# Optimization experiments

Measured on AMD Instinct MI355X. Metric: run time of the kernel, lower is better.

Reference implementation:

```python
import jax, jax.numpy as jnp
import numpy as np

B, H, W, DM = 4, 64, 64, 96
DS, DC, K = 16, 3, 4
DI = DM            # expand = 1.0
DTR = 6            # ceil(96/16)


def setup_inputs() -> dict:
    key = jax.random.key(0)
    ks = jax.random.split(key, 12)
    s = 0.02
    # dt bias init exactly as MS2D.dt_init: dt ~ exp(U*(log(max)-log(min))+log(min)); inv softplus
    dt = jnp.exp(jax.random.uniform(ks[5], (K, DI)) * (np.log(0.1) - np.log(0.001)) + np.log(0.001))
    dt = jnp.clip(dt, 1e-4, None)
    inv_dt = dt + jnp.log(-jnp.expm1(-dt))
    A_logs = jnp.log(jnp.broadcast_to(jnp.arange(1, DS + 1, dtype=jnp.float32), (K, DI, DS)))
    return {
        "x": jax.random.normal(ks[0], (B, H, W, DM), jnp.float32),
        "in_proj_w": jax.random.normal(ks[1], (2 * DI, DM), jnp.float32) * s,
        "conv_w": jax.random.normal(ks[2], (DI, 1, DC, DC), jnp.float32) * s,
        "conv_b": jnp.zeros((DI,), jnp.float32),
        "x_proj_weight": jax.random.normal(ks[3], (K, DTR + 2 * DS, DI), jnp.float32) * s,
        "dt_projs_weight": jax.random.uniform(ks[4], (K, DI, DTR), minval=-1.0, maxval=1.0) * (DTR ** -0.5),
        "dt_projs_bias": inv_dt,
        "A_logs": A_logs,
        "Ds": jnp.ones((K, DI), jnp.float32),
        "out_norm_w": jnp.ones((DI,), jnp.float32),
        "out_norm_b": jnp.zeros((DI,), jnp.float32),
        "out_proj_w": jax.random.normal(ks[6], (DM, DI), jnp.float32) * s,
    }


def _ms2d(x, in_proj_w, conv_w, conv_b, x_proj_weight, dt_projs_weight,
          dt_projs_bias, A_logs, Ds, out_norm_w, out_norm_b, out_proj_w):
    Bb, Hh, Ww, _ = x.shape
    L = Hh * Ww
    # in_proj -> (x, z) gating split
    xz = x @ in_proj_w.T                      # (B,H,W,2*DI)
    xc, z = jnp.split(xz, 2, axis=-1)
    xc = jnp.transpose(xc, (0, 3, 1, 2))      # (B,DI,H,W)
    xc = jax.lax.conv_general_dilated(
        xc, conv_w, (1, 1), 'SAME', feature_group_count=xc.shape[1],
        dimension_numbers=('NCHW', 'OIHW', 'NCHW')) + conv_b[None, :, None, None]
    xc = jax.nn.silu(xc)
    d = xc.shape[1]
    # 4-directional scan sequences: hw, wh, and their reverses
    x_hw = xc.reshape(Bb, d, L)
    x_wh = jnp.transpose(xc, (0, 1, 3, 2)).reshape(Bb, d, L)
    x2 = jnp.stack([x_hw, x_wh], axis=1)          # (B,2,d,L)
    xs = jnp.concatenate([x2, jnp.flip(x2, axis=-1)], axis=1)  # (B,4,d,L)
    x_dbl = jnp.einsum('bkdl,kcd->bkcl', xs, x_proj_weight)
    dtr = dt_projs_weight.shape[2]
    n = A_logs.shape[2]
    dts, Bs, Cs = jnp.split(x_dbl, [dtr, dtr + n], axis=2)     # (B,4,r,L),(B,4,N,L),(B,4,N,L)
    dts = jnp.einsum('bkrl,kdr->bkdl', dts, dt_projs_weight)
    delta = jax.nn.softplus(dts + dt_projs_bias[None, :, :, None])  # (B,4,d,L)
    A = -jnp.exp(A_logs)                                        # (4,d,N)
    # time-major for scan
    u_t = jnp.moveaxis(xs, -1, 0)       # (L,B,4,d)
    dl_t = jnp.moveaxis(delta, -1, 0)
    B_t = jnp.moveaxis(Bs, -1, 0)       # (L,B,4,N)
    C_t = jnp.moveaxis(Cs, -1, 0)

    def step(h, inp):                   # h: (B,4,d,N)
        u, dl, b, c = inp
        dA = jnp.exp(dl[..., None] * A)
        h = h * dA + (dl * u)[..., None] * b[:, :, None, :]
        y = jnp.einsum('bkdn,bkn->bkd', h, c)
        return h, y

    h0 = jnp.zeros((Bb, 4, d, n), xs.dtype)
    _, ys = jax.lax.scan(step, h0, (u_t, dl_t, B_t, C_t))
    ys = jnp.moveaxis(ys, 0, -1)        # (B,4,d,L)
    ys = ys + Ds[None, :, :, None] * xs  # skip D*u
    inv_y = jnp.flip(ys[:, 2:4], axis=-1)

    def wh2hw(t):  # undo the (W,H) raster order
        return jnp.transpose(t.reshape(Bb, d, Ww, Hh), (0, 1, 3, 2)).reshape(Bb, d, L)

    y = ys[:, 0] + inv_y[:, 0] + wh2hw(ys[:, 1]) + wh2hw(inv_y[:, 1])
    y = jnp.transpose(y, (0, 2, 1)).reshape(Bb, Hh, Ww, d)
    mu = y.mean(-1, keepdims=True)
    var = y.var(-1, keepdims=True)
    y = (y - mu) / jnp.sqrt(var + 1e-5) * out_norm_w + out_norm_b
    y = y * jax.nn.silu(z)
    return y @ out_proj_w.T


def reference(x, in_proj_w, conv_w, conv_b, x_proj_weight, dt_projs_weight,
              dt_projs_bias, A_logs, Ds, out_norm_w, out_norm_b, out_proj_w):
    return _ms2d(x, in_proj_w, conv_w, conv_b, x_proj_weight, dt_projs_weight,
                 dt_projs_bias, A_logs, Ds, out_norm_w, out_norm_b, out_proj_w)
```

## Files before the change

kernel.cpp:

```cpp
#include <hip/hip_runtime.h>
#include <math.h>


#define LQ 4096
#define NCH 128
#define LCH 32

__device__ __forceinline__ float sigmoid_f(float x){ return 1.0f/(1.0f + __expf(-x)); }
__device__ __forceinline__ float silu_f(float x){ return x * sigmoid_f(x); }
__device__ __forceinline__ float softplus_f(float x){ return (x > 20.0f) ? x : __logf(1.0f + __expf(x)); }

__device__ __forceinline__ int pos_of(int k, int i){
  switch(k & 3){
    case 0: return i;
    case 1: return ((i & 63) << 6) | (i >> 6);
    case 2: return LQ - 1 - i;
    default: { int j = LQ - 1 - i; return ((j & 63) << 6) | (j >> 6); }
  }
}

__device__ __forceinline__ void pow8(float r, int nh, float* e){
  e[0]=r; e[1]=r*r; e[2]=e[1]*r; e[3]=e[1]*e[1];
  e[4]=e[3]*r; e[5]=e[3]*e[1]; e[6]=e[3]*e[2]; e[7]=e[3]*e[3];
  float m = nh ? e[7] : 1.0f;
  #pragma unroll
  for (int j=0;j<8;j++) e[j] *= m;
}

__global__ __launch_bounds__(64) void k_prep(const float* __restrict__ Alogs,
                                             float* __restrict__ An_tab,
                                             float* __restrict__ fflag){
  const int t = blockIdx.x*64 + threadIdx.x;
  if (t >= 384) return;
  bool fast = true;
  #pragma unroll
  for (int n=0;n<16;n++){
    float An = -__expf(Alogs[t*16+n]);
    An_tab[t*16+n] = An;
    fast = fast && (fabsf(An + (float)(n+1)) < 1e-3f*(float)(n+1));
  }
  fflag[t] = fast ? 1.0f : 0.0f;
}

__global__ __launch_bounds__(256) void k_inproj(const float* __restrict__ x,
                                                const float* __restrict__ wproj,
                                                float* __restrict__ xc,
                                                float* __restrict__ zb){
  __shared__ float a_s[64*97];
  __shared__ float w_s[96*97];
  const int t = threadIdx.x;
  const int row0 = (blockIdx.x >> 1) * 64;
  const int ch = blockIdx.x & 1;
  for (int e = t*4; e < 64*96; e += 1024){
    float4 v = *(const float4*)(x + (size_t)row0*96 + e);
    int r = e/96, c = e%96;
    float* p = a_s + r*97 + c;
    p[0]=v.x; p[1]=v.y; p[2]=v.z; p[3]=v.w;
  }
  for (int e = t*4; e < 96*96; e += 1024){
    float4 v = *(const float4*)(wproj + (size_t)ch*96*96 + e);
    int r = e/96, c = e%96;
    float* p = w_s + r*97 + c;
    p[0]=v.x; p[1]=v.y; p[2]=v.z; p[3]=v.w;
  }
  __syncthreads();
  const int tr = t >> 5, tc = t & 31;
  float acc[8][3];
  #pragma unroll
  for (int i=0;i<8;i++){
    #pragma unroll
    for (int j=0;j<3;j++) acc[i][j]=0.f;
  }
  for (int kk=0; kk<96; kk++){
    float a[8], b[3];
    #pragma unroll
    for (int i=0;i<8;i++) a[i] = a_s[(tr*8+i)*97+kk];
    #pragma unroll
    for (int j=0;j<3;j++) b[j] = w_s[(tc*3+j)*97+kk];
    #pragma unroll
    for (int i=0;i<8;i++){
      #pragma unroll
      for (int j=0;j<3;j++) acc[i][j] += a[i]*b[j];
    }
  }
  float* dst = ch ? zb : xc;
  #pragma unroll
  for (int i=0;i<8;i++){
    int row = row0 + tr*8 + i;
    #pragma unroll
    for (int j=0;j<3;j++) dst[(size_t)row*96 + tc*3 + j] = acc[i][j];
  }
}

__global__ __launch_bounds__(256) void k_conv(const float* __restrict__ xc,
                                              const float* __restrict__ cw,
                                              const float* __restrict__ cb,
                                              float* __restrict__ u){
  int e = blockIdx.x*256 + threadIdx.x;
  int d0 = (e % 24) * 4;
  int p = e / 24;
  int w = p & 63, h = (p >> 6) & 63, b = p >> 12;
  float cwv[4][9];
  #pragma unroll
  for (int q=0;q<4;q++){
    #pragma unroll
    for (int tp=0;tp<9;tp++) cwv[q][tp] = cw[(d0+q)*9+tp];
  }
  float4 acc = make_float4(cb[d0], cb[d0+1], cb[d0+2], cb[d0+3]);
  #pragma unroll
  for (int kh=0; kh<3; kh++){
    int hh = h + kh - 1;
    if (hh < 0 || hh > 63) continue;
    #pragma unroll
    for (int kw=0; kw<3; kw++){
      int ww = w + kw - 1;
      if (ww < 0 || ww > 63) continue;
      float4 v = *(const float4*)(xc + ((size_t)((b<<12) + (hh<<6) + ww))*96 + d0);
      int tp = kh*3+kw;
      acc.x += v.x*cwv[0][tp]; acc.y += v.y*cwv[1][tp];
      acc.z += v.z*cwv[2][tp]; acc.w += v.w*cwv[3][tp];
    }
  }
  float4 o = make_float4(silu_f(acc.x), silu_f(acc.y), silu_f(acc.z), silu_f(acc.w));
  *(float4*)(u + (size_t)p*96 + d0) = o;
}

__global__ __launch_bounds__(128) void k_proj(const float* __restrict__ u,
                                              const float* __restrict__ xpw,
                                              float* __restrict__ dts,
                                              float* __restrict__ Bsb,
                                              float* __restrict__ Csb,
                                              float* __restrict__ us){
  __shared__ float u_s[64*97];
  __shared__ float w_s[40*97];
  const int t = threadIdx.x;
  const int blk = blockIdx.x;
  const int pt = blk & 63, k = (blk >> 6) & 3, b = blk >> 8;
  const int bk = b*4 + k;
  const int i0 = pt * 64;
  for (int e = t*4; e < 64*96; e += 512){
    int row = e/96, c = e%96;
    int p = pos_of(k, i0 + row);
    float4 v = *(const float4*)(u + ((size_t)((b<<12) + p))*96 + c);
    float* dst = u_s + row*97 + c;
    dst[0]=v.x; dst[1]=v.y; dst[2]=v.z; dst[3]=v.w;
    if (us) *(float4*)(us + ((size_t)((bk<<12) + i0 + row))*96 + c) = v;
  }
  for (int e = t*4; e < 40*96; e += 512){
    int r = e/96, c = e%96;
    float4 v = (r < 38) ? *(const float4*)(xpw + (k*38+r)*96 + c)
                        : make_float4(0,0,0,0);
    float* p = w_s + r*97 + c;
    p[0]=v.x; p[1]=v.y; p[2]=v.z; p[3]=v.w;
  }
  __syncthreads();
  const int posg = t & 15, cg = t >> 4;
  float acc[4][5];
  #pragma unroll
  for (int i=0;i<4;i++){
    #pragma unroll
    for (int j=0;j<5;j++) acc[i][j]=0.f;
  }
  for (int dd=0; dd<96; dd++){
    float uu[4], wv[5];
    #pragma unroll
    for (int i=0;i<4;i++) uu[i] = u_s[(posg*4+i)*97+dd];
    #pragma unroll
    for (int j=0;j<5;j++) wv[j] = w_s[(cg*5+j)*97+dd];
    #pragma unroll
    for (int i=0;i<4;i++){
      #pragma unroll
      for (int j=0;j<5;j++) acc[i][j] += uu[i]*wv[j];
    }
  }
  #pragma unroll
  for (int i=0;i<4;i++){
    int ii = i0 + posg*4 + i;
    int base = (bk<<12) + ii;
    #pragma unroll
    for (int j=0;j<5;j++){
      int c = cg*5 + j;
      float v = acc[i][j];
      if (c < 6)       dts[(size_t)base*6 + c] = v;
      else if (c < 22) Bsb[(size_t)base*16 + (c-6)] = v;
      else if (c < 38) Csb[(size_t)base*16 + (c-22)] = v;
    }
  }
}

__global__ __launch_bounds__(384) void k_scanA2(float* us,
                                                const float* __restrict__ dts,
                                                const float* __restrict__ Bsb,
                                                const float* __restrict__ Csb,
                                                const float* __restrict__ dtw_g,
                                                const float* __restrict__ dtb_g,
                                                const float* __restrict__ An_tab,
                                                const float* __restrict__ fflag,
                                                float* __restrict__ S,
                                                float* __restrict__ sumd,
                                                float* __restrict__ ys){
  const int t = threadIdx.x;
  const int c2 = t / 192;
  const int lane = t & 63;
  const int wv3 = (t % 192) >> 6;
  const int nh = (lane >> 5) & 1;
  const int d = wv3*32 + (lane & 31);
  const int blk = blockIdx.x;
  const int bk = blk >> 6;
  const int k = bk & 3;
  const int chunk = ((blk & 63) << 1) | c2;
  const int ibase = chunk * LCH;
  int wfast = __all(fflag[k*96+d] > 0.5f ? 1 : 0);
  float An[8];
  #pragma unroll
  for (int j=0;j<8;j++) An[j] = An_tab[(k*96+d)*16 + nh*8 + j];
  float dtw[6];
  #pragma unroll
  for (int r=0;r<6;r++) dtw[r] = dtw_g[(k*96+d)*6+r];
  const float bias = dtb_g[k*96+d];
  float* usp = us + ((size_t)((bk<<12)+ibase))*96 + d;
  const float2* dtp = (const float2*)(dts + ((size_t)((bk<<12)+ibase))*6);
  const float4* Bp = (const float4*)(Bsb + ((size_t)((bk<<12)+ibase))*16) + nh*2;
  const float4* Cp = (const float4*)(Csb + ((size_t)((bk<<12)+ibase))*16) + nh*2;
  float* yp = ys + ((size_t)((bk<<12)+ibase))*96 + d;
  float h[8];
  #pragma unroll
  for (int n=0;n<8;n++) h[n]=0.f;
  float cum = 0.f;
  if (wfast){
    #pragma unroll 8
    for (int il=0; il<LCH; il++){
      float uv = usp[(size_t)il*96];
      float2 q0 = dtp[il*3+0], q1 = dtp[il*3+1], q2 = dtp[il*3+2];
      float accd = bias + dtw[0]*q0.x + dtw[1]*q0.y + dtw[2]*q1.x
                        + dtw[3]*q1.y + dtw[4]*q2.x + dtw[5]*q2.y;
      float t1 = __expf(accd);
      float r = 1.0f / (1.0f + t1);
      float delta = (accd > 20.f) ? accd : __logf(1.0f + t1);
      cum += delta;
      float du = delta * uv;
      float4 b0 = Bp[il*4+0], b1 = Bp[il*4+1];
      float4 c0 = Cp[il*4+0], c1 = Cp[il*4+1];
      float Bv[8] = {b0.x,b0.y,b0.z,b0.w, b1.x,b1.y,b1.z,b1.w};
      float Cv[8] = {c0.x,c0.y,c0.z,c0.w, c1.x,c1.y,c1.z,c1.w};
      float e[8];
      pow8(r, nh, e);
      float y8 = 0.f;
      #pragma unroll
      for (int n=0;n<8;n++){
        h[n] = h[n]*e[n] + du*Bv[n];
        y8 += h[n]*Cv[n];
      }
      float y = y8 + __shfl_xor(y8, 32, 64);
      if (nh == 0){ yp[(size_t)il*96] = y; usp[(size_t)il*96] = cum; }
    }
  } else {
    #pragma unroll 2
    for (int il=0; il<LCH; il++){
      float uv = usp[(size_t)il*96];
      float2 q0 = dtp[il*3+0], q1 = dtp[il*3+1], q2 = dtp[il*3+2];
      float accd = bias + dtw[0]*q0.x + dtw[1]*q0.y + dtw[2]*q1.x
                        + dtw[3]*q1.y + dtw[4]*q2.x + dtw[5]*q2.y;
      float delta = softplus_f(accd);
      cum += delta;
      float du = delta * uv;
      float4 b0 = Bp[il*4+0], b1 = Bp[il*4+1];
      float4 c0 = Cp[il*4+0], c1 = Cp[il*4+1];
      float Bv[8] = {b0.x,b0.y,b0.z,b0.w, b1.x,b1.y,b1.z,b1.w};
      float Cv[8] = {c0.x,c0.y,c0.z,c0.w, c1.x,c1.y,c1.z,c1.w};
      float e[8];
      #pragma unroll
      for (int n=0;n<8;n++) e[n] = __expf(delta*An[n]);
      float y8 = 0.f;
      #pragma unroll
      for (int n=0;n<8;n++){
        h[n] = h[n]*e[n] + du*Bv[n];
        y8 += h[n]*Cv[n];
      }
      float y = y8 + __shfl_xor(y8, 32, 64);
      if (nh == 0){ yp[(size_t)il*96] = y; usp[(size_t)il*96] = cum; }
    }
  }
  const int sb = (bk*NCH + chunk)*96 + d;
  float4* Sp = (float4*)(S + (size_t)sb*16 + nh*8);
  Sp[0] = make_float4(h[0],h[1],h[2],h[3]);
  Sp[1] = make_float4(h[4],h[5],h[6],h[7]);
  if (nh == 0) sumd[sb] = cum;
}

__global__ __launch_bounds__(384) void k_scanA_fb(const float* __restrict__ u,
                                                  const float* __restrict__ dts,
                                                  const float* __restrict__ Bsb,
                                                  const float* __restrict__ dtw_g,
                                                  const float* __restrict__ dtb_g,
                                                  const float* __restrict__ Alogs,
                                                  float* __restrict__ S,
                                                  float* __restrict__ sumd){
  const int t = threadIdx.x;
  const int c2 = t / 192;
  const int lane = t & 63;
  const int wv3 = (t % 192) >> 6;
  const int nh = (lane >> 5) & 1;
  const int d = wv3*32 + (lane & 31);
  const int blk = blockIdx.x;
  const int bk = blk >> 6;
  const int k = bk & 3, b = bk >> 2;
  const int chunk = ((blk & 63) << 1) | c2;
  const int ibase = chunk * LCH;
  float An[8];
  bool fast = true;
  #pragma unroll
  for (int j=0;j<8;j++){
    int n = nh*8 + j;
    An[j] = -__expf(Alogs[(k*96+d)*16+n]);
    fast = fast && (fabsf(An[j] + (float)(n+1)) < 1e-3f*(float)(n+1));
  }
  int wfast = __all(fast ? 1 : 0);
  float dtw[6];
  #pragma unroll
  for (int r=0;r<6;r++) dtw[r] = dtw_g[(k*96+d)*6+r];
  const float bias = dtb_g[k*96+d];
  int pb = pos_of(k, ibase);
  int pstep = pos_of(k, ibase+1) - pb;
  const float* uptr = u + ((size_t)((b<<12)+pb))*96 + d;
  const long ustep = (long)pstep*96;
  const float2* dtp = (const float2*)(dts + ((size_t)((bk<<12)+ibase))*6);
  const float4* Bp = (const float4*)(Bsb + ((size_t)((bk<<12)+ibase))*16) + nh*2;
  float h[8];
  #pragma unroll
  for (int n=0;n<8;n++) h[n]=0.f;
  float sdelta = 0.f;
  #pragma unroll 4
  for (int il=0; il<LCH; il++){
    float uv = *uptr;
    float2 q0 = dtp[0], q1 = dtp[1], q2 = dtp[2];
    float accd = bias + dtw[0]*q0.x + dtw[1]*q0.y + dtw[2]*q1.x
                      + dtw[3]*q1.y + dtw[4]*q2.x + dtw[5]*q2.y;
    float t1 = __expf(accd);
    float r = 1.0f / (1.0f + t1);
    float delta = (accd > 20.f) ? accd : __logf(1.0f + t1);
    sdelta += delta;
    float du = delta * uv;
    float4 b0 = Bp[0], b1 = Bp[1];
    float Bv[8] = {b0.x,b0.y,b0.z,b0.w, b1.x,b1.y,b1.z,b1.w};
    float e[8];
    if (wfast){ pow8(r, nh, e); }
    else {
      #pragma unroll
      for (int n=0;n<8;n++) e[n] = __expf(delta*An[n]);
    }
    #pragma unroll
    for (int n=0;n<8;n++) h[n] = h[n]*e[n] + du*Bv[n];
    uptr += ustep; dtp += 3; Bp += 4;
  }
  const int sb = (bk*NCH + chunk)*96 + d;
  float4* Sp = (float4*)(S + (size_t)sb*16 + nh*8);
  Sp[0] = make_float4(h[0],h[1],h[2],h[3]);
  Sp[1] = make_float4(h[4],h[5],h[6],h[7]);
  if (nh == 0) sumd[sb] = sdelta;
}

__global__ __launch_bounds__(128) void k_scanB2(float* __restrict__ S,
                                                const float* __restrict__ sumd,
                                                const float* __restrict__ Alogs,
                                                const float* __restrict__ An_tab,
                                                const float* __restrict__ fflag){
  __shared__ float As[128*17];
  __shared__ float Bs[128*17];
  const int c = threadIdx.x;
  const int blk = blockIdx.x;
  const int d = blk % 96;
  const int bk = blk / 96;
  const int k = bk & 3;
  const int sb = (bk*NCH + c)*96 + d;
  float a[16], bvals[16];
  {
    const float4* Sp = (const float4*)(S + (size_t)sb*16);
    float4 s0=Sp[0], s1=Sp[1], s2=Sp[2], s3=Sp[3];
    bvals[0]=s0.x;bvals[1]=s0.y;bvals[2]=s0.z;bvals[3]=s0.w;
    bvals[4]=s1.x;bvals[5]=s1.y;bvals[6]=s1.z;bvals[7]=s1.w;
    bvals[8]=s2.x;bvals[9]=s2.y;bvals[10]=s2.z;bvals[11]=s2.w;
    bvals[12]=s3.x;bvals[13]=s3.y;bvals[14]=s3.z;bvals[15]=s3.w;
  }
  const float sd = sumd[sb];
  bool fast;
  float An[16];
  if (An_tab){
    fast = fflag[k*96+d] > 0.5f;
    if (!fast){
      #pragma unroll
      for (int n=0;n<16;n++) An[n] = An_tab[(k*96+d)*16+n];
    }
  } else {
    fast = true;
    #pragma unroll
    for (int n=0;n<16;n++){
      An[n] = -__expf(Alogs[(k*96+d)*16+n]);
      fast = fast && (fabsf(An[n] + (float)(n+1)) < 1e-3f*(float)(n+1));
    }
  }
  if (fast){
    float q = __expf(-sd);
    float p = q;
    #pragma unroll
    for (int n=0;n<16;n++){ a[n] = p; p *= q; }
  } else {
    #pragma unroll
    for (int n=0;n<16;n++) a[n] = __expf(An[n]*sd);
  }
  #pragma unroll
  for (int n=0;n<16;n++){ As[c*17+n] = a[n]; Bs[c*17+n] = bvals[n]; }
  for (int dist=1; dist<128; dist<<=1){
    __syncthreads();
    float aL[16], bL[16];
    if (c >= dist){
      #pragma unroll
      for (int n=0;n<16;n++){ aL[n] = As[(c-dist)*17+n]; bL[n] = Bs[(c-dist)*17+n]; }
    }
    __syncthreads();
    if (c >= dist){
      #pragma unroll
      for (int n=0;n<16;n++){
        bvals[n] = bL[n]*a[n] + bvals[n];
        a[n] = aL[n]*a[n];
        As[c*17+n] = a[n]; Bs[c*17+n] = bvals[n];
      }
    }
  }
  __syncthreads();
  float h0[16];
  #pragma unroll
  for (int n=0;n<16;n++) h0[n] = (c == 0) ? 0.f : Bs[(c-1)*17+n];
  float4* Sp = (float4*)(S + (size_t)sb*16);
  Sp[0] = make_float4(h0[0],h0[1],h0[2],h0[3]);
  Sp[1] = make_float4(h0[4],h0[5],h0[6],h0[7]);
  Sp[2] = make_float4(h0[8],h0[9],h0[10],h0[11]);
  Sp[3] = make_float4(h0[12],h0[13],h0[14],h0[15]);
}

__global__ __launch_bounds__(256) void k_scanY(const float* __restrict__ us,
                                               const float* __restrict__ Csb,
                                               const float* __restrict__ An_tab,
                                               const float* __restrict__ fflag,
                                               const float* __restrict__ h0buf,
                                               float* __restrict__ ys){
  __shared__ float h0_s[32*17];
  __shared__ float An_s[32*17];
  __shared__ float ff_s[32];
  const int t = threadIdx.x;
  const int blk = blockIdx.x;
  const int dslice = blk % 3;
  const int tmp = blk / 3;
  const int chunk = tmp & 127;
  const int bk = tmp >> 7;
  const int k = bk & 3;
  const int dbase = dslice * 32;
  {
    const float* h0src = h0buf + ((size_t)((bk*NCH + chunk)*96 + dbase))*16;
    const float* Ansrc = An_tab + (size_t)(k*96 + dbase)*16;
    for (int e = t; e < 512; e += 256){
      int dl = e >> 4, n = e & 15;
      h0_s[dl*17+n] = h0src[e];
      An_s[dl*17+n] = Ansrc[e];
    }
    if (t < 32) ff_s[t] = fflag[k*96 + dbase + t];
  }
  __syncthreads();
  const int il = t >> 3;
  const int dq = t & 7;
  const int d0 = dbase + dq*4;
  const int i = chunk*LCH + il;
  const size_t rowb = (size_t)((bk<<12) + i);
  float4 cd = *(const float4*)(us + rowb*96 + d0);
  float4 yl = *(const float4*)(ys + rowb*96 + d0);
  float Cv[16];
  {
    const float4* Cp = (const float4*)(Csb + rowb*16);
    float4 c0=Cp[0], c1=Cp[1], c2=Cp[2], c3=Cp[3];
    Cv[0]=c0.x;Cv[1]=c0.y;Cv[2]=c0.z;Cv[3]=c0.w;
    Cv[4]=c1.x;Cv[5]=c1.y;Cv[6]=c1.z;Cv[7]=c1.w;
    Cv[8]=c2.x;Cv[9]=c2.y;Cv[10]=c2.z;Cv[11]=c2.w;
    Cv[12]=c3.x;Cv[13]=c3.y;Cv[14]=c3.z;Cv[15]=c3.w;
  }
  float yout[4] = {yl.x, yl.y, yl.z, yl.w};
  float cdv[4] = {cd.x, cd.y, cd.z, cd.w};
  #pragma unroll
  for (int dd=0; dd<4; dd++){
    const int dl = dq*4 + dd;
    float acc = 0.f;
    if (ff_s[dl] > 0.5f){
      float q = __expf(-cdv[dd]);
      float p = q;
      #pragma unroll
      for (int n=0;n<16;n++){ acc += Cv[n]*h0_s[dl*17+n]*p; p *= q; }
    } else {
      #pragma unroll
      for (int n=0;n<16;n++) acc += Cv[n]*h0_s[dl*17+n]*__expf(An_s[dl*17+n]*cdv[dd]);
    }
    yout[dd] += acc;
  }
  *(float4*)(ys + rowb*96 + d0) = make_float4(yout[0], yout[1], yout[2], yout[3]);
}

__global__ __launch_bounds__(384) void k_scanC_fb(const float* __restrict__ u,
                                                  const float* __restrict__ dts,
                                                  const float* __restrict__ Bsb,
                                                  const float* __restrict__ Csb,
                                                  const float* __restrict__ dtw_g,
                                                  const float* __restrict__ dtb_g,
                                                  const float* __restrict__ Alogs,
                                                  const float* __restrict__ h0buf,
                                                  float* __restrict__ ys){
  const int t = threadIdx.x;
  const int c2 = t / 192;
  const int lane = t & 63;
  const int wv3 = (t % 192) >> 6;
  const int nh = (lane >> 5) & 1;
  const int d = wv3*32 + (lane & 31);
  const int blk = blockIdx.x;
  const int bk = blk >> 6;
  const int k = bk & 3, b = bk >> 2;
  const int chunk = ((blk & 63) << 1) | c2;
  const int ibase = chunk * LCH;
  float An[8];
  bool fast = true;
  #pragma unroll
  for (int j=0;j<8;j++){
    int n = nh*8 + j;
    An[j] = -__expf(Alogs[(k*96+d)*16+n]);
    fast = fast && (fabsf(An[j] + (float)(n+1)) < 1e-3f*(float)(n+1));
  }
  int wfast = __all(fast ? 1 : 0);
  float dtw[6];
  #pragma unroll
  for (int r=0;r<6;r++) dtw[r] = dtw_g[(k*96+d)*6+r];
  const float bias = dtb_g[k*96+d];
  int pb = pos_of(k, ibase);
  int pstep = pos_of(k, ibase+1) - pb;
  const float* uptr = u + ((size_t)((b<<12)+pb))*96 + d;
  const long ustep = (long)pstep*96;
  const float2* dtp = (const float2*)(dts + ((size_t)((bk<<12)+ibase))*6);
  const float4* Bp = (const float4*)(Bsb + ((size_t)((bk<<12)+ibase))*16) + nh*2;
  const float4* Cp = (const float4*)(Csb + ((size_t)((bk<<12)+ibase))*16) + nh*2;
  float* yp = ys + ((size_t)((bk<<12)+ibase))*96 + d;
  float h[8];
  const int sb = (bk*NCH + chunk)*96 + d;
  const float4* Hp = (const float4*)(h0buf + (size_t)sb*16 + nh*8);
  {
    float4 h0=Hp[0], h1=Hp[1];
    h[0]=h0.x;h[1]=h0.y;h[2]=h0.z;h[3]=h0.w;
    h[4]=h1.x;h[5]=h1.y;h[6]=h1.z;h[7]=h1.w;
  }
  #pragma unroll 4
  for (int il=0; il<LCH; il++){
    float uv = *uptr;
    float2 q0 = dtp[0], q1 = dtp[1], q2 = dtp[2];
    float accd = bias + dtw[0]*q0.x + dtw[1]*q0.y + dtw[2]*q1.x
                      + dtw[3]*q1.y + dtw[4]*q2.x + dtw[5]*q2.y;
    float t1 = __expf(accd);
    float r = 1.0f / (1.0f + t1);
    float delta = (accd > 20.f) ? accd : __logf(1.0f + t1);
    float du = delta * uv;
    float4 b0 = Bp[0], b1 = Bp[1];
    float4 c0 = Cp[0], c1 = Cp[1];
    float Bv[8] = {b0.x,b0.y,b0.z,b0.w, b1.x,b1.y,b1.z,b1.w};
    float Cv[8] = {c0.x,c0.y,c0.z,c0.w, c1.x,c1.y,c1.z,c1.w};
    float e[8];
    if (wfast){ pow8(r, nh, e); }
    else {
      #pragma unroll
      for (int n=0;n<8;n++) e[n] = __expf(delta*An[n]);
    }
    float y8 = 0.f;
    #pragma unroll
    for (int n=0;n<8;n++){
      h[n] = h[n]*e[n] + du*Bv[n];
      y8 += h[n]*Cv[n];
    }
    float y = y8 + __shfl_xor(y8, 32, 64);
    if (nh == 0) yp[(size_t)il*96] = y;
    uptr += ustep; dtp += 3; Bp += 4; Cp += 4;
  }
}

__global__ __launch_bounds__(256) void k_out(const float* __restrict__ ys,
                                             const float* __restrict__ ubuf,
                                             const float* __restrict__ Dsg,
                                             const float* __restrict__ zbuf,
                                             const float* __restrict__ nw,
                                             const float* __restrict__ nb,
                                             const float* __restrict__ wout,
                                             float* __restrict__ out){
  __shared__ float w_s[96*97];
  __shared__ float g_s[32*97];
  const int t = threadIdx.x;
  const int b = blockIdx.x >> 7;
  const int pt = blockIdx.x & 127;
  const int p0 = pt * 32;
  for (int e=t*4; e<96*96; e+=1024){
    float4 v = *(const float4*)(wout+e);
    int r=e/96, c=e%96;
    float* p = w_s + r*97 + c;
    p[0]=v.x; p[1]=v.y; p[2]=v.z; p[3]=v.w;
  }
  const int pos = t >> 3, lane8 = t & 7, d0 = lane8*12;
  const int p = p0 + pos;
  const int tp = ((p & 63) << 6) | (p >> 6);
  int idx[4];
  idx[0] = p; idx[1] = tp; idx[2] = LQ-1-p; idx[3] = LQ-1-tp;
  float yv[12];
  float s1=0.f, s2=0.f;
  #pragma unroll
  for (int i=0;i<12;i+=4){
    float4 a = make_float4(0,0,0,0);
    #pragma unroll
    for (int kk=0;kk<4;kk++){
      float4 v = *(const float4*)(ys + ((size_t)(((b*4+kk)<<12) + idx[kk]))*96 + d0 + i);
      a.x+=v.x; a.y+=v.y; a.z+=v.z; a.w+=v.w;
    }
    float4 uv = *(const float4*)(ubuf + ((size_t)((b<<12)+p))*96 + d0 + i);
    #pragma unroll
    for (int q=0;q<4;q++){
      int dd = d0+i+q;
      float sD = Dsg[dd] + Dsg[96+dd] + Dsg[192+dd] + Dsg[288+dd];
      float uq = (q==0)?uv.x:(q==1)?uv.y:(q==2)?uv.z:uv.w;
      float* aq = (q==0)?&a.x:(q==1)?&a.y:(q==2)?&a.z:&a.w;
      *aq += sD * uq;
    }
    yv[i]=a.x; yv[i+1]=a.y; yv[i+2]=a.z; yv[i+3]=a.w;
    s1 += a.x+a.y+a.z+a.w;
    s2 += a.x*a.x + a.y*a.y + a.z*a.z + a.w*a.w;
  }
  #pragma unroll
  for (int m=1; m<8; m<<=1){
    s1 += __shfl_xor(s1, m, 64);
    s2 += __shfl_xor(s2, m, 64);
  }
  const float mu = s1 * (1.0f/96.0f);
  const float var = s2 * (1.0f/96.0f) - mu*mu;
  const float rstd = rsqrtf(var + 1e-5f);
  #pragma unroll
  for (int i=0;i<12;i+=4){
    float4 zv = *(const float4*)(zbuf + ((size_t)((b<<12)+p))*96 + d0 + i);
    float zz[4] = {zv.x,zv.y,zv.z,zv.w};
    #pragma unroll
    for (int q=0;q<4;q++){
      int d = d0+i+q;
      float yn = (yv[i+q]-mu)*rstd*nw[d] + nb[d];
      g_s[pos*97 + d] = yn * silu_f(zz[q]);
    }
  }
  __syncthreads();
  const int posg = t >> 5, mg = t & 31;
  float acc[4][3];
  #pragma unroll
  for (int i=0;i<4;i++){
    #pragma unroll
    for (int j=0;j<3;j++) acc[i][j]=0.f;
  }
  for (int dd=0; dd<96; dd++){
    float g4[4], w3[3];
    #pragma unroll
    for (int i=0;i<4;i++) g4[i] = g_s[(posg*4+i)*97+dd];
    #pragma unroll
    for (int j=0;j<3;j++) w3[j] = w_s[(mg*3+j)*97+dd];
    #pragma unroll
    for (int i=0;i<4;i++){
      #pragma unroll
      for (int j=0;j<3;j++) acc[i][j] += g4[i]*w3[j];
    }
  }
  #pragma unroll
  for (int i=0;i<4;i++){
    int prow = p0 + posg*4 + i;
    #pragma unroll
    for (int j=0;j<3;j++){
      out[((size_t)((b<<12)+prow))*96 + mg*3 + j] = acc[i][j];
    }
  }
}

extern "C" void kernel_launch(void* const* d_in, const int* in_sizes, int n_in,
                              void* d_out, int out_size, void* d_ws, size_t ws_size,
                              hipStream_t stream) {
  (void)in_sizes; (void)n_in; (void)out_size;
  const float* x   = (const float*)d_in[0];
  const float* ipw = (const float*)d_in[1];
  const float* cw  = (const float*)d_in[2];
  const float* cb  = (const float*)d_in[3];
  const float* xpw = (const float*)d_in[4];
  const float* dtw = (const float*)d_in[5];
  const float* dtb = (const float*)d_in[6];
  const float* alg = (const float*)d_in[7];
  const float* dsg = (const float*)d_in[8];
  const float* nw  = (const float*)d_in[9];
  const float* nb  = (const float*)d_in[10];
  const float* wo  = (const float*)d_in[11];
  float* out = (float*)d_out;

  float* w = (float*)d_ws;
  size_t off = 0;
  float* z_b    = w + off; off += 1572864;
  float* u_b    = w + off; off += 1572864;
  float* dts_b  = w + off; off += 393216;
  float* Bs_b   = w + off; off += 1048576;
  float* Cs_b   = w + off; off += 1048576;
  float* Sh_b   = w + off; off += 3145728;
  float* ys_b   = w + off; off += 6291456;
  float* xc_b   = ys_b;
  size_t need_primary = (off + 196608 + 6291456 + 6144 + 384) * sizeof(float);
  float* sumd_ded = w + off;
  float* us_b     = sumd_ded + 196608;
  float* antab_b  = us_b + 6291456;
  float* fflag_b  = antab_b + 6144;
  bool primary = (ws_size >= need_primary);
  float* sumd_b = primary ? sumd_ded : ys_b;

  if (primary) k_prep<<<6, 64, 0, stream>>>(alg, antab_b, fflag_b);
  k_inproj<<<512, 256, 0, stream>>>(x, ipw, xc_b, z_b);
  k_conv  <<<1536, 256, 0, stream>>>(xc_b, cw, cb, u_b);
  k_proj  <<<1024, 128, 0, stream>>>(u_b, xpw, dts_b, Bs_b, Cs_b, primary ? us_b : nullptr);
  if (primary){
    k_scanA2<<<1024, 384, 0, stream>>>(us_b, dts_b, Bs_b, Cs_b, dtw, dtb,
                                       antab_b, fflag_b, Sh_b, sumd_b, ys_b);
    k_scanB2<<<1536, 128, 0, stream>>>(Sh_b, sumd_b, alg, antab_b, fflag_b);
    k_scanY <<<6144, 256, 0, stream>>>(us_b, Cs_b, antab_b, fflag_b, Sh_b, ys_b);
  } else {
    k_scanA_fb<<<1024, 384, 0, stream>>>(u_b, dts_b, Bs_b, dtw, dtb, alg, Sh_b, sumd_b);
    k_scanB2<<<1536, 128, 0, stream>>>(Sh_b, sumd_b, alg, nullptr, nullptr);
    k_scanC_fb<<<1024, 384, 0, stream>>>(u_b, dts_b, Bs_b, Cs_b, dtw, dtb, alg, Sh_b, ys_b);
  }
  k_out   <<<512, 256, 0, stream>>>(ys_b, u_b, dsg, z_b, nw, nb, wo, out);
}
```

Before: 234.4 us.

## Give each scan thread all 16 states and software-prefetch next step's inputs

The chunked scan kernel now has one thread own a full 16-element state per channel instead of splitting it across two half-waves. This removes the cross-lane shuffle, the half-idle stores and the duplicated dt/softplus work. It also prefetches the next timestep's u, dt, B and C into registers to hide load latency, and halves the block size to 192 threads. In exchange it uses more registers per thread, launches half as many threads (192 per block, with waves that straddle the two chunks), and leaves less thread-level parallelism to hide the serial dependency.

```diff
diff --git a/kernel.cpp b/kernel.cpp
--- a/kernel.cpp
+++ b/kernel.cpp
@@ -25,6 +25,13 @@
   float m = nh ? e[7] : 1.0f;
   #pragma unroll
   for (int j=0;j<8;j++) e[j] *= m;
+}
+
+__device__ __forceinline__ void pow16(float r, float* e){
+  e[0]=r; e[1]=r*r; e[2]=e[1]*r; e[3]=e[1]*e[1];
+  e[4]=e[3]*r; e[5]=e[3]*e[1]; e[6]=e[3]*e[2]; e[7]=e[3]*e[3];
+  e[8]=e[7]*r; e[9]=e[7]*e[1]; e[10]=e[7]*e[2]; e[11]=e[7]*e[3];
+  e[12]=e[7]*e[4]; e[13]=e[7]*e[5]; e[14]=e[7]*e[6]; e[15]=e[7]*e[7];
 }
 
 __global__ __launch_bounds__(64) void k_prep(const float* __restrict__ Alogs,
@@ -188,7 +195,7 @@
   }
 }
 
-__global__ __launch_bounds__(384) void k_scanA2(float* us,
+__global__ __launch_bounds__(192, 3) void k_scanA2(float* us,
                                                 const float* __restrict__ dts,
                                                 const float* __restrict__ Bsb,
                                                 const float* __restrict__ Csb,
@@ -200,92 +207,116 @@
                                                 float* __restrict__ sumd,
                                                 float* __restrict__ ys){
   const int t = threadIdx.x;
-  const int c2 = t / 192;
-  const int lane = t & 63;
-  const int wv3 = (t % 192) >> 6;
-  const int nh = (lane >> 5) & 1;
-  const int d = wv3*32 + (lane & 31);
+  const int d = t % 96;
+  const int c2 = t / 96;
   const int blk = blockIdx.x;
   const int bk = blk >> 6;
   const int k = bk & 3;
   const int chunk = ((blk & 63) << 1) | c2;
   const int ibase = chunk * LCH;
-  int wfast = __all(fflag[k*96+d] > 0.5f ? 1 : 0);
-  float An[8];
-  #pragma unroll
-  for (int j=0;j<8;j++) An[j] = An_tab[(k*96+d)*16 + nh*8 + j];
+  const int kd = k*96 + d;
+  int wfast = __all(fflag[kd] > 0.5f ? 1 : 0);
   float dtw[6];
   #pragma unroll
-  for (int r=0;r<6;r++) dtw[r] = dtw_g[(k*96+d)*6+r];
-  const float bias = dtb_g[k*96+d];
+  for (int r=0;r<6;r++) dtw[r] = dtw_g[kd*6+r];
+  const float bias = dtb_g[kd];
   float* usp = us + ((size_t)((bk<<12)+ibase))*96 + d;
-  const float2* dtp = (const float2*)(dts + ((size_t)((bk<<12)+ibase))*6);
-  const float4* Bp = (const float4*)(Bsb + ((size_t)((bk<<12)+ibase))*16) + nh*2;
-  const float4* Cp = (const float4*)(Csb + ((size_t)((bk<<12)+ibase))*16) + nh*2;
+  const float* dtp = dts + ((size_t)((bk<<12)+ibase))*6;
+  const float4* Bp = (const float4*)(Bsb + ((size_t)((bk<<12)+ibase))*16);
+  const float4* Cp = (const float4*)(Csb + ((size_t)((bk<<12)+ibase))*16);
   float* yp = ys + ((size_t)((bk<<12)+ibase))*96 + d;
-  float h[8];
-  #pragma unroll
-  for (int n=0;n<8;n++) h[n]=0.f;
+  float h[16];
+  #pragma unroll
+  for (int n=0;n<16;n++) h[n]=0.f;
   float cum = 0.f;
+  float u_n = usp[0];
+  float2 q0n = *(const float2*)(dtp+0);
+  float2 q1n = *(const float2*)(dtp+2);
+  float2 q2n = *(const float2*)(dtp+4);
+  float4 B0n=Bp[0], B1n=Bp[1], B2n=Bp[2], B3n=Bp[3];
+  float4 C0n=Cp[0], C1n=Cp[1], C2n=Cp[2], C3n=Cp[3];
   if (wfast){
-    #pragma unroll 8
+    #pragma unroll 4
     for (int il=0; il<LCH; il++){
-      float uv = usp[(size_t)il*96];
-      float2 q0 = dtp[il*3+0], q1 = dtp[il*3+1], q2 = dtp[il*3+2];
+      float u_c = u_n;
+      float2 q0=q0n, q1=q1n, q2=q2n;
+      float4 B0=B0n,B1=B1n,B2=B2n,B3=B3n;
+      float4 C0=C0n,C1=C1n,C2=C2n,C3=C3n;
+      int nx = (il+1 < LCH) ? il+1 : il;
+      u_n = usp[(size_t)nx*96];
+      q0n = *(const float2*)(dtp+nx*6);
+      q1n = *(const float2*)(dtp+nx*6+2);
+      q2n = *(const float2*)(dtp+nx*6+4);
+      B0n=Bp[nx*4+0]; B1n=Bp[nx*4+1]; B2n=Bp[nx*4+2]; B3n=Bp[nx*4+3];
+      C0n=Cp[nx*4+0]; C1n=Cp[nx*4+1]; C2n=Cp[nx*4+2]; C3n=Cp[nx*4+3];
       float accd = bias + dtw[0]*q0.x + dtw[1]*q0.y + dtw[2]*q1.x
                         + dtw[3]*q1.y + dtw[4]*q2.x + dtw[5]*q2.y;
       float t1 = __expf(accd);
-      float r = 1.0f / (1.0f + t1);
+      float r = 1.0f/(1.0f+t1);
       float delta = (accd > 20.f) ? accd : __logf(1.0f + t1);
       cum += delta;
-      float du = delta * uv;
-      float4 b0 = Bp[il*4+0], b1 = Bp[il*4+1];
-      float4 c0 = Cp[il*4+0], c1 = Cp[il*4+1];
-      float Bv[8] = {b0.x,b0.y,b0.z,b0.w, b1.x,b1.y,b1.z,b1.w};
-      float Cv[8] = {c0.x,c0.y,c0.z,c0.w, c1.x,c1.y,c1.z,c1.w};
-      float e[8];
-      pow8(r, nh, e);
-      float y8 = 0.f;
-      #pragma unroll
-      for (int n=0;n<8;n++){
+      float du = delta * u_c;
+      float Bv[16] = {B0.x,B0.y,B0.z,B0.w, B1.x,B1.y,B1.z,B1.w,
+                      B2.x,B2.y,B2.z,B2.w, B3.x,B3.y,B3.z,B3.w};
+      float Cv[16] = {C0.x,C0.y,C0.z,C0.w, C1.x,C1.y,C1.z,C1.w,
+                      C2.x,C2.y,C2.z,C2.w, C3.x,C3.y,C3.z,C3.w};
+      float e[16];
+      pow16(r, e);
+      float y = 0.f;
+      #pragma unroll
+      for (int n=0;n<16;n++){
         h[n] = h[n]*e[n] + du*Bv[n];
-        y8 += h[n]*Cv[n];
+        y += h[n]*Cv[n];
       }
-      float y = y8 + __shfl_xor(y8, 32, 64);
-      if (nh == 0){ yp[(size_t)il*96] = y; usp[(size_t)il*96] = cum; }
+      yp[(size_t)il*96] = y;
+      usp[(size_t)il*96] = cum;
     }
   } else {
+    float An[16];
+    #pragma unroll
+    for (int n=0;n<16;n++) An[n] = An_tab[kd*16+n];
     #pragma unroll 2
     for (int il=0; il<LCH; il++){
-      float uv = usp[(size_t)il*96];
-      float2 q0 = dtp[il*3+0], q1 = dtp[il*3+1], q2 = dtp[il*3+2];
+      float u_c = u_n;
+      float2 q0=q0n, q1=q1n, q2=q2n;
+      float4 B0=B0n,B1=B1n,B2=B2n,B3=B3n;
+      float4 C0=C0n,C1=C1n,C2=C2n,C3=C3n;
+      int nx = (il+1 < LCH) ? il+1 : il;
+      u_n = usp[(size_t)nx*96];
+      q0n = *(const float2*)(dtp+nx*6);
+      q1n = *(const float2*)(dtp+nx*6+2);
+      q2n = *(const float2*)(dtp+nx*6+4);
+      B0n=Bp[nx*4+0]; B1n=Bp[nx*4+1]; B2n=Bp[nx*4+2]; B3n=Bp[nx*4+3];
+      C0n=Cp[nx*4+0]; C1n=Cp[nx*4+1]; C2n=Cp[nx*4+2]; C3n=Cp[nx*4+3];
       float accd = bias + dtw[0]*q0.x + dtw[1]*q0.y + dtw[2]*q1.x
                         + dtw[3]*q1.y + dtw[4]*q2.x + dtw[5]*q2.y;
       float delta = softplus_f(accd);
       cum += delta;
-      float du = delta * uv;
-      float4 b0 = Bp[il*4+0], b1 = Bp[il*4+1];
-      float4 c0 = Cp[il*4+0], c1 = Cp[il*4+1];
-      float Bv[8] = {b0.x,b0.y,b0.z,b0.w, b1.x,b1.y,b1.z,b1.w};
-      float Cv[8] = {c0.x,c0.y,c0.z,c0.w, c1.x,c1.y,c1.z,c1.w};
-      float e[8];
-      #pragma unroll
-      for (int n=0;n<8;n++) e[n] = __expf(delta*An[n]);
-      float y8 = 0.f;
-      #pragma unroll
-      for (int n=0;n<8;n++){
+      float du = delta * u_c;
+      float Bv[16] = {B0.x,B0.y,B0.z,B0.w, B1.x,B1.y,B1.z,B1.w,
+                      B2.x,B2.y,B2.z,B2.w, B3.x,B3.y,B3.z,B3.w};
+      float Cv[16] = {C0.x,C0.y,C0.z,C0.w, C1.x,C1.y,C1.z,C1.w,
+                      C2.x,C2.y,C2.z,C2.w, C3.x,C3.y,C3.z,C3.w};
+      float e[16];
+      #pragma unroll
+      for (int n=0;n<16;n++) e[n] = __expf(delta*An[n]);
+      float y = 0.f;
+      #pragma unroll
+      for (int n=0;n<16;n++){
         h[n] = h[n]*e[n] + du*Bv[n];
-        y8 += h[n]*Cv[n];
+        y += h[n]*Cv[n];
       }
-      float y = y8 + __shfl_xor(y8, 32, 64);
-      if (nh == 0){ yp[(size_t)il*96] = y; usp[(size_t)il*96] = cum; }
+      yp[(size_t)il*96] = y;
+      usp[(size_t)il*96] = cum;
     }
   }
   const int sb = (bk*NCH + chunk)*96 + d;
-  float4* Sp = (float4*)(S + (size_t)sb*16 + nh*8);
+  float4* Sp = (float4*)(S + (size_t)sb*16);
   Sp[0] = make_float4(h[0],h[1],h[2],h[3]);
   Sp[1] = make_float4(h[4],h[5],h[6],h[7]);
-  if (nh == 0) sumd[sb] = cum;
+  Sp[2] = make_float4(h[8],h[9],h[10],h[11]);
+  Sp[3] = make_float4(h[12],h[13],h[14],h[15]);
+  sumd[sb] = cum;
 }
 
 __global__ __launch_bounds__(384) void k_scanA_fb(const float* __restrict__ u,
@@ -721,7 +752,7 @@
   k_conv  <<<1536, 256, 0, stream>>>(xc_b, cw, cb, u_b);
   k_proj  <<<1024, 128, 0, stream>>>(u_b, xpw, dts_b, Bs_b, Cs_b, primary ? us_b : nullptr);
   if (primary){
-    k_scanA2<<<1024, 384, 0, stream>>>(us_b, dts_b, Bs_b, Cs_b, dtw, dtb,
+    k_scanA2<<<1024, 192, 0, stream>>>(us_b, dts_b, Bs_b, Cs_b, dtw, dtb,
                                        antab_b, fflag_b, Sh_b, sumd_b, ys_b);
     k_scanB2<<<1536, 128, 0, stream>>>(Sh_b, sumd_b, alg, antab_b, fflag_b);
     k_scanY <<<6144, 256, 0, stream>>>(us_b, Cs_b, antab_b, fflag_b, Sh_b, ys_b);
```

Result: slower. 249.3 us (+6.4%).

## Drop permuted u copy in k_proj; gather u directly in scan with prefetch

Applied to the files above, without the earlier changes.

k_proj no longer writes a per-direction permuted copy of u (a 6M-float buffer). k_scanA2 now reads u straight from the spatial layout through pos_of with a fixed per-chunk stride, and writes the cumulative delta to a separate buffer instead of overwriting us. The scan loop also software-prefetches the next step's u, dt, B and C values, and gets a launch-bounds occupancy hint with a smaller unroll. This removes a large global write and avoids reusing the buffer in place. The cost is strided, transposed reads of u for the column-order directions and higher register pressure from the prefetch.

```diff
diff --git a/kernel.cpp b/kernel.cpp
--- a/kernel.cpp
+++ b/kernel.cpp
@@ -129,8 +129,7 @@
                                               const float* __restrict__ xpw,
                                               float* __restrict__ dts,
                                               float* __restrict__ Bsb,
-                                              float* __restrict__ Csb,
-                                              float* __restrict__ us){
+                                              float* __restrict__ Csb){
   __shared__ float u_s[64*97];
   __shared__ float w_s[40*97];
   const int t = threadIdx.x;
@@ -144,7 +143,6 @@
     float4 v = *(const float4*)(u + ((size_t)((b<<12) + p))*96 + c);
     float* dst = u_s + row*97 + c;
     dst[0]=v.x; dst[1]=v.y; dst[2]=v.z; dst[3]=v.w;
-    if (us) *(float4*)(us + ((size_t)((bk<<12) + i0 + row))*96 + c) = v;
   }
   for (int e = t*4; e < 40*96; e += 512){
     int r = e/96, c = e%96;
@@ -188,7 +186,7 @@
   }
 }
 
-__global__ __launch_bounds__(384) void k_scanA2(float* us,
+__global__ __launch_bounds__(384, 2) void k_scanA2(const float* __restrict__ u,
                                                 const float* __restrict__ dts,
                                                 const float* __restrict__ Bsb,
                                                 const float* __restrict__ Csb,
@@ -198,7 +196,8 @@
                                                 const float* __restrict__ fflag,
                                                 float* __restrict__ S,
                                                 float* __restrict__ sumd,
-                                                float* __restrict__ ys){
+                                                float* __restrict__ ys,
+                                                float* __restrict__ cum_g){
   const int t = threadIdx.x;
   const int c2 = t / 192;
   const int lane = t & 63;
@@ -207,42 +206,55 @@
   const int d = wv3*32 + (lane & 31);
   const int blk = blockIdx.x;
   const int bk = blk >> 6;
-  const int k = bk & 3;
+  const int k = bk & 3, b = bk >> 2;
   const int chunk = ((blk & 63) << 1) | c2;
   const int ibase = chunk * LCH;
-  int wfast = __all(fflag[k*96+d] > 0.5f ? 1 : 0);
+  const int kd = k*96 + d;
+  int wfast = __all(fflag[kd] > 0.5f ? 1 : 0);
   float An[8];
   #pragma unroll
-  for (int j=0;j<8;j++) An[j] = An_tab[(k*96+d)*16 + nh*8 + j];
+  for (int j=0;j<8;j++) An[j] = An_tab[kd*16 + nh*8 + j];
   float dtw[6];
   #pragma unroll
-  for (int r=0;r<6;r++) dtw[r] = dtw_g[(k*96+d)*6+r];
-  const float bias = dtb_g[k*96+d];
-  float* usp = us + ((size_t)((bk<<12)+ibase))*96 + d;
+  for (int r=0;r<6;r++) dtw[r] = dtw_g[kd*6+r];
+  const float bias = dtb_g[kd];
+  const int pb = pos_of(k, ibase);
+  const int pstep = pos_of(k, ibase+1) - pb;
+  const float* uptr = u + ((size_t)((b<<12)+pb))*96 + d;
+  const long ustep = (long)pstep*96;
   const float2* dtp = (const float2*)(dts + ((size_t)((bk<<12)+ibase))*6);
   const float4* Bp = (const float4*)(Bsb + ((size_t)((bk<<12)+ibase))*16) + nh*2;
   const float4* Cp = (const float4*)(Csb + ((size_t)((bk<<12)+ibase))*16) + nh*2;
   float* yp = ys + ((size_t)((bk<<12)+ibase))*96 + d;
+  float* cp = cum_g + ((size_t)((bk<<12)+ibase))*96 + d;
   float h[8];
   #pragma unroll
   for (int n=0;n<8;n++) h[n]=0.f;
   float cum = 0.f;
+  float u_n = uptr[0];
+  float2 q0n = dtp[0], q1n = dtp[1], q2n = dtp[2];
+  float4 B0n = Bp[0], B1n = Bp[1];
+  float4 C0n = Cp[0], C1n = Cp[1];
   if (wfast){
-    #pragma unroll 8
+    #pragma unroll 4
     for (int il=0; il<LCH; il++){
-      float uv = usp[(size_t)il*96];
-      float2 q0 = dtp[il*3+0], q1 = dtp[il*3+1], q2 = dtp[il*3+2];
+      float u_c = u_n;
+      float2 q0=q0n, q1=q1n, q2=q2n;
+      float4 B0=B0n, B1=B1n, C0=C0n, C1=C1n;
+      const int nx = (il+1 < LCH) ? il+1 : il;
+      u_n = uptr[(long)nx*ustep];
+      q0n = dtp[nx*3+0]; q1n = dtp[nx*3+1]; q2n = dtp[nx*3+2];
+      B0n = Bp[nx*4+0]; B1n = Bp[nx*4+1];
+      C0n = Cp[nx*4+0]; C1n = Cp[nx*4+1];
       float accd = bias + dtw[0]*q0.x + dtw[1]*q0.y + dtw[2]*q1.x
                         + dtw[3]*q1.y + dtw[4]*q2.x + dtw[5]*q2.y;
       float t1 = __expf(accd);
-      float r = 1.0f / (1.0f + t1);
+      float r = 1.0f/(1.0f+t1);
       float delta = (accd > 20.f) ? accd : __logf(1.0f + t1);
       cum += delta;
-      float du = delta * uv;
-      float4 b0 = Bp[il*4+0], b1 = Bp[il*4+1];
-      float4 c0 = Cp[il*4+0], c1 = Cp[il*4+1];
-      float Bv[8] = {b0.x,b0.y,b0.z,b0.w, b1.x,b1.y,b1.z,b1.w};
-      float Cv[8] = {c0.x,c0.y,c0.z,c0.w, c1.x,c1.y,c1.z,c1.w};
+      float du = delta * u_c;
+      float Bv[8] = {B0.x,B0.y,B0.z,B0.w, B1.x,B1.y,B1.z,B1.w};
+      float Cv[8] = {C0.x,C0.y,C0.z,C0.w, C1.x,C1.y,C1.z,C1.w};
       float e[8];
       pow8(r, nh, e);
       float y8 = 0.f;
@@ -252,22 +264,26 @@
         y8 += h[n]*Cv[n];
       }
       float y = y8 + __shfl_xor(y8, 32, 64);
-      if (nh == 0){ yp[(size_t)il*96] = y; usp[(size_t)il*96] = cum; }
+      if (nh == 0){ yp[(size_t)il*96] = y; cp[(size_t)il*96] = cum; }
     }
   } else {
     #pragma unroll 2
     for (int il=0; il<LCH; il++){
-      float uv = usp[(size_t)il*96];
-      float2 q0 = dtp[il*3+0], q1 = dtp[il*3+1], q2 = dtp[il*3+2];
+      float u_c = u_n;
+      float2 q0=q0n, q1=q1n, q2=q2n;
+      float4 B0=B0n, B1=B1n, C0=C0n, C1=C1n;
+      const int nx = (il+1 < LCH) ? il+1 : il;
+      u_n = uptr[(long)nx*ustep];
+      q0n = dtp[nx*3+0]; q1n = dtp[nx*3+1]; q2n = dtp[nx*3+2];
+      B0n = Bp[nx*4+0]; B1n = Bp[nx*4+1];
+      C0n = Cp[nx*4+0]; C1n = Cp[nx*4+1];
       float accd = bias + dtw[0]*q0.x + dtw[1]*q0.y + dtw[2]*q1.x
                         + dtw[3]*q1.y + dtw[4]*q2.x + dtw[5]*q2.y;
       float delta = softplus_f(accd);
       cum += delta;
-      float du = delta * uv;
-      float4 b0 = Bp[il*4+0], b1 = Bp[il*4+1];
-      float4 c0 = Cp[il*4+0], c1 = Cp[il*4+1];
-      float Bv[8] = {b0.x,b0.y,b0.z,b0.w, b1.x,b1.y,b1.z,b1.w};
-      float Cv[8] = {c0.x,c0.y,c0.z,c0.w, c1.x,c1.y,c1.z,c1.w};
+      float du = delta * u_c;
+      float Bv[8] = {B0.x,B0.y,B0.z,B0.w, B1.x,B1.y,B1.z,B1.w};
+      float Cv[8] = {C0.x,C0.y,C0.z,C0.w, C1.x,C1.y,C1.z,C1.w};
       float e[8];
       #pragma unroll
       for (int n=0;n<8;n++) e[n] = __expf(delta*An[n]);
@@ -278,7 +294,7 @@
         y8 += h[n]*Cv[n];
       }
       float y = y8 + __shfl_xor(y8, 32, 64);
-      if (nh == 0){ yp[(size_t)il*96] = y; usp[(size_t)il*96] = cum; }
+      if (nh == 0){ yp[(size_t)il*96] = y; cp[(size_t)il*96] = cum; }
     }
   }
   const int sb = (bk*NCH + chunk)*96 + d;
@@ -438,7 +454,7 @@
   Sp[3] = make_float4(h0[12],h0[13],h0[14],h0[15]);
 }
 
-__global__ __launch_bounds__(256) void k_scanY(const float* __restrict__ us,
+__global__ __launch_bounds__(256) void k_scanY(const float* __restrict__ cum_g,
                                                const float* __restrict__ Csb,
                                                const float* __restrict__ An_tab,
                                                const float* __restrict__ fflag,
@@ -471,7 +487,7 @@
   const int d0 = dbase + dq*4;
   const int i = chunk*LCH + il;
   const size_t rowb = (size_t)((bk<<12) + i);
-  float4 cd = *(const float4*)(us + rowb*96 + d0);
+  float4 cd = *(const float4*)(cum_g + rowb*96 + d0);
   float4 yl = *(const float4*)(ys + rowb*96 + d0);
   float Cv[16];
   {
@@ -710,8 +726,8 @@
   float* xc_b   = ys_b;
   size_t need_primary = (off + 196608 + 6291456 + 6144 + 384) * sizeof(float);
   float* sumd_ded = w + off;
-  float* us_b     = sumd_ded + 196608;
-  float* antab_b  = us_b + 6291456;
+  float* cum_b    = sumd_ded + 196608;
+  float* antab_b  = cum_b + 6291456;
   float* fflag_b  = antab_b + 6144;
   bool primary = (ws_size >= need_primary);
   float* sumd_b = primary ? sumd_ded : ys_b;
@@ -719,12 +735,12 @@
   if (primary) k_prep<<<6, 64, 0, stream>>>(alg, antab_b, fflag_b);
   k_inproj<<<512, 256, 0, stream>>>(x, ipw, xc_b, z_b);
   k_conv  <<<1536, 256, 0, stream>>>(xc_b, cw, cb, u_b);
-  k_proj  <<<1024, 128, 0, stream>>>(u_b, xpw, dts_b, Bs_b, Cs_b, primary ? us_b : nullptr);
+  k_proj  <<<1024, 128, 0, stream>>>(u_b, xpw, dts_b, Bs_b, Cs_b);
   if (primary){
-    k_scanA2<<<1024, 384, 0, stream>>>(us_b, dts_b, Bs_b, Cs_b, dtw, dtb,
-                                       antab_b, fflag_b, Sh_b, sumd_b, ys_b);
+    k_scanA2<<<1024, 384, 0, stream>>>(u_b, dts_b, Bs_b, Cs_b, dtw, dtb,
+                                       antab_b, fflag_b, Sh_b, sumd_b, ys_b, cum_b);
     k_scanB2<<<1536, 128, 0, stream>>>(Sh_b, sumd_b, alg, antab_b, fflag_b);
-    k_scanY <<<6144, 256, 0, stream>>>(us_b, Cs_b, antab_b, fflag_b, Sh_b, ys_b);
+    k_scanY <<<6144, 256, 0, stream>>>(cum_b, Cs_b, antab_b, fflag_b, Sh_b, ys_b);
   } else {
     k_scanA_fb<<<1024, 384, 0, stream>>>(u_b, dts_b, Bs_b, dtw, dtb, alg, Sh_b, sumd_b);
     k_scanB2<<<1536, 128, 0, stream>>>(Sh_b, sumd_b, alg, nullptr, nullptr);
```

Result: no change. 230.6 us (-1.6%).
